# Kernel tuning notes

Hardware: AMD Instinct MI355X
Metric: run time of the kernel (lower is better)

Reference implementation:

```python
import jax, jax.numpy as jnp
import numpy as np

NUM_HEADS = 16
D_MODEL = 1024
HEAD_DIM = D_MODEL // NUM_HEADS
NEG_BIG = 1e10


def setup_inputs() -> dict:
    key = jax.random.key(0)
    k1, k2, k3 = jax.random.split(key, 3)
    B, T = 2, 2048
    from_tensor = jax.random.normal(k1, (B, T, D_MODEL), dtype=jnp.float32)
    init = 0.02
    Wqkv = jax.random.normal(k2, (D_MODEL, 3 * D_MODEL), dtype=jnp.float32) * init
    bqkv = jnp.zeros((3 * D_MODEL,), dtype=jnp.float32)
    Wproj = jax.random.normal(k3, (D_MODEL, D_MODEL), dtype=jnp.float32) * init
    bproj = jnp.zeros((D_MODEL,), dtype=jnp.float32)
    return {"from_tensor": from_tensor, "Wqkv": Wqkv, "bqkv": bqkv,
            "Wproj": Wproj, "bproj": bproj}


def reference(from_tensor, Wqkv, bqkv, Wproj, bproj):
    B, T, D = from_tensor.shape
    H, hd = NUM_HEADS, D // NUM_HEADS
    qkv = from_tensor @ Wqkv + bqkv                      # [B,T,3D]
    q, k, v = jnp.split(qkv, 3, axis=-1)
    def heads(x):  # [B,T,D] -> [B,H,T,hd]
        return x.reshape(B, T, H, hd).transpose(0, 2, 1, 3)
    q, k, v = heads(q), heads(k), heads(v)
    present = jnp.stack([k, v], axis=1)                  # [B,2,H,T,hd]
    scores = jnp.einsum('bhqd,bhkd->bhqk', q, k)         # [B,H,T,T]
    scores = scores * jax.lax.rsqrt(jnp.float32(hd))
    # faithful mask: m = i > j - ns + nd (strict; diagonal masked)
    nd = ns = T
    i = jnp.arange(nd)[:, None]
    j = jnp.arange(ns)
    m = (i > j - ns + nd).astype(scores.dtype)           # [T,T]
    scores = scores * m - NEG_BIG * (1.0 - m)
    probs = jax.nn.softmax(scores, axis=-1)
    ctx = jnp.einsum('bhqk,bhkd->bhqd', probs, v)        # [B,H,T,hd]
    ctx = ctx.transpose(0, 2, 1, 3).reshape(B, T, D)
    out = ctx @ Wproj + bproj                            # [B,T,D]
    return out, present
```

## Files before the change

### kernel.cpp

```cpp
#include <hip/hip_runtime.h>
#include <hip/hip_bf16.h>
#include <cstdint>

typedef __bf16 bf16_t;
typedef __bf16 bf16x4 __attribute__((ext_vector_type(4)));
typedef __bf16 bf16x8 __attribute__((ext_vector_type(8)));
typedef float  f32x4  __attribute__((ext_vector_type(4)));

#define MFMA16(a,b,c) __builtin_amdgcn_mfma_f32_16x16x32_bf16(a,b,c,0,0,0)

#if __has_builtin(__builtin_amdgcn_exp2f)
#define EXP2(x) __builtin_amdgcn_exp2f(x)
#else
#define EXP2(x) exp2f(x)
#endif

__device__ __forceinline__ void gl_lds16(const void* g, void* l){
    __builtin_amdgcn_global_load_lds(
        (const __attribute__((address_space(1))) void*)g,
        (__attribute__((address_space(3))) void*)l, 16, 0, 0);
}

__global__ void k_cvt(const float* __restrict__ src, bf16_t* __restrict__ dst, int n4){
    int stride = gridDim.x * blockDim.x;
    for (int i = blockIdx.x * blockDim.x + threadIdx.x; i < n4; i += stride){
        float4 v = ((const float4*)src)[i];
        bf16x4 o = { (bf16_t)v.x, (bf16_t)v.y, (bf16_t)v.z, (bf16_t)v.w };
        ((bf16x4*)dst)[i] = o;
    }
}

__global__ void k_transpose_cvt(const float* __restrict__ src, bf16_t* __restrict__ dst,
                                int R, int C){
    __shared__ bf16_t tile[32][33];
    int c0 = blockIdx.x * 32, r0 = blockIdx.y * 32;
    int tx = threadIdx.x & 31, g = threadIdx.x >> 5;
#pragma unroll
    for (int p = 0; p < 4; ++p){
        int r = g + p * 8;
        tile[r][tx] = (bf16_t)src[(size_t)(r0 + r) * C + c0 + tx];
    }
    __syncthreads();
#pragma unroll
    for (int p = 0; p < 4; ++p){
        int rr = g + p * 8;
        dst[(size_t)(c0 + rr) * R + r0 + tx] = tile[tx][rr];
    }
}

template<int MODE>
__global__ void k_gemm(const bf16_t* __restrict__ A, const bf16_t* __restrict__ Bt,
                       const float* __restrict__ bias,
                       float* __restrict__ Cout,
                       bf16_t* __restrict__ qws, bf16_t* __restrict__ kws,
                       bf16_t* __restrict__ vws,
                       int M, int N, int K){
    __shared__ bf16_t sA[128 * 64];
    __shared__ bf16_t sB[128 * 64];
    int m0 = blockIdx.x * 128, n0 = blockIdx.y * 128;
    int tid = threadIdx.x, lane = tid & 63, w = tid >> 6;
    int lr = lane & 15, lg = lane >> 4;
    int wm = (w >> 1) * 64, wn = (w & 1) * 64;
    f32x4 acc[4][4] = {};

    int srow = lane >> 3;
    int scol = ((lane & 7) ^ srow) * 8;

    for (int k0 = 0; k0 < K; k0 += 64){
#pragma unroll
        for (int p = 0; p < 4; ++p){
            int c = w + p * 4;
            gl_lds16(A  + (size_t)(m0 + c * 8 + srow) * K + k0 + scol, &sA[c * 512]);
            gl_lds16(Bt + (size_t)(n0 + c * 8 + srow) * K + k0 + scol, &sB[c * 512]);
        }
        __syncthreads();
#pragma unroll
        for (int ks = 0; ks < 2; ++ks){
            bf16x8 af[4], bfm[4];
            int ca = ((ks * 4 + lg) ^ (lr & 7)) * 8;
#pragma unroll
            for (int i = 0; i < 4; ++i){
                af[i]  = *(const bf16x8*)(sA + (wm + i * 16 + lr) * 64 + ca);
                bfm[i] = *(const bf16x8*)(sB + (wn + i * 16 + lr) * 64 + ca);
            }
            __builtin_amdgcn_s_setprio(1);
#pragma unroll
            for (int i = 0; i < 4; ++i)
#pragma unroll
                for (int j = 0; j < 4; ++j)
                    acc[i][j] = MFMA16(bfm[j], af[i], acc[i][j]);
            __builtin_amdgcn_s_setprio(0);
        }
        __syncthreads();
    }

#pragma unroll
    for (int j = 0; j < 4; ++j){
        int nb = n0 + wn + j * 16 + lg * 4;
        f32x4 bv = *(const f32x4*)(bias + nb);
#pragma unroll
        for (int i = 0; i < 4; ++i){
            int m = m0 + wm + i * 16 + lr;
            f32x4 cv = acc[i][j];
            cv[0] += bv[0]; cv[1] += bv[1]; cv[2] += bv[2]; cv[3] += bv[3];
            if (MODE == 1){
                *(f32x4*)(Cout + (size_t)m * N + nb) = cv;
            } else {
                int b = m >> 11, t = m & 2047;
                int sec = nb >> 10, rem = nb & 1023;
                int h = rem >> 6, d = rem & 63;
                size_t hbase = (((size_t)b * 16 + h) * 2048 + t) * 64;
                if (sec == 0){
                    bf16x4 qv = {(bf16_t)cv[0], (bf16_t)cv[1], (bf16_t)cv[2], (bf16_t)cv[3]};
                    *(bf16x4*)(qws + hbase + d) = qv;
                } else if (sec == 1){
                    bf16x4 kv = {(bf16_t)cv[0], (bf16_t)cv[1], (bf16_t)cv[2], (bf16_t)cv[3]};
                    *(bf16x4*)(kws + hbase + (d ^ ((t & 7) << 3))) = kv;
                    *(f32x4*)(Cout + ((((size_t)b * 2 + 0) * 16 + h) * 2048 + t) * 64 + d) = cv;
                } else {
                    *(f32x4*)(Cout + ((((size_t)b * 2 + 1) * 16 + h) * 2048 + t) * 64 + d) = cv;
                    int tl = t & 63;
                    int sp = (tl & 0x23) | ((tl & 0x0C) << 1) | ((tl & 0x10) >> 2);
#pragma unroll
                    for (int r = 0; r < 4; ++r){
                        int dd = d + r;
                        vws[(((size_t)b * 16 + h) * 64 + dd) * 2048 + (t & ~63)
                            + (sp ^ ((dd & 7) << 3))] = (bf16_t)cv[r];
                    }
                }
            }
        }
    }
}

__device__ __forceinline__ void stage_kv8(const bf16_t* khead, const bf16_t* vhead,
                                          bf16_t* sKb, bf16_t* sVb,
                                          int kv0, int w, int lane){
    gl_lds16(khead + (size_t)(kv0 + w * 8 + (lane >> 3)) * 64 + (lane & 7) * 8,
             sKb + w * 512);
    gl_lds16(vhead + (size_t)(w * 8 + (lane >> 3)) * 2048 + kv0 + (lane & 7) * 8,
             sVb + w * 512);
}

__global__ __launch_bounds__(512, 4) void k_flash(const bf16_t* __restrict__ qb,
                        const bf16_t* __restrict__ kb, const bf16_t* __restrict__ vt,
                        bf16_t* __restrict__ ctx){
    __shared__ bf16_t sK[3][4096];
    __shared__ bf16_t sV[3][4096];
    int bid = blockIdx.x;
    int x = bid & 7, p = bid >> 3;
    int c = p & 31, pass = p >> 5;
    int bh = x * 4 + pass * 2 + (c >> 4);
    int qt = pass ? 15 - (c & 15) : (c & 15);
    int b = bh >> 4, h = bh & 15;
    int tid = threadIdx.x, lane = tid & 63, w = tid >> 6;
    int lr = lane & 15, lg = lane >> 4;
    int q0 = qt * 128;
    int nkt = 2 * qt + 2;
    const bf16_t* qhead = qb + (size_t)bh * 131072;
    const bf16_t* khead = kb + (size_t)bh * 131072;
    const bf16_t* vhead = vt + (size_t)bh * 131072;
    const float SC = 0.18033688f;

    bf16x8 aq0, aq1;
    {
        const bf16_t* p2 = qhead + (size_t)(q0 + w * 16 + lr) * 64 + lg * 8;
        bf16x8 r0 = *(const bf16x8*)p2, r1 = *(const bf16x8*)(p2 + 32);
#pragma unroll
        for (int j = 0; j < 8; ++j){
            aq0[j] = (bf16_t)((float)r0[j] * SC);
            aq1[j] = (bf16_t)((float)r1[j] * SC);
        }
    }
    float lsum = 0.f;
    f32x4 oacc[4] = {};

    bf16_t *cK = sK[0], *cV = sV[0];
    bf16_t *nK = sK[1], *nV = sV[1];
    bf16_t *xK = sK[2], *xV = sV[2];
    stage_kv8(khead, vhead, cK, cV, 0, w, lane);
    stage_kv8(khead, vhead, nK, nV, 64, w, lane);

    for (int kt = 0; kt < nkt; ++kt){
        asm volatile("s_waitcnt vmcnt(2)" ::: "memory");
        __builtin_amdgcn_s_barrier();
        {
            int nt = kt + 2; if (nt > nkt - 1) nt = nkt - 1;
            stage_kv8(khead, vhead, xK, xV, nt * 64, w, lane);
        }

        bf16x8 kf[8], vf[8];
#pragma unroll
        for (int cf = 0; cf < 4; ++cf){
            kf[cf * 2]     = *(const bf16x8*)(&cK[(cf * 16 + lr) * 64 + ((lg * 8) ^ ((lr & 7) << 3))]);
            kf[cf * 2 + 1] = *(const bf16x8*)(&cK[(cf * 16 + lr) * 64 + ((32 + lg * 8) ^ ((lr & 7) << 3))]);
        }
#pragma unroll
        for (int ks = 0; ks < 2; ++ks)
#pragma unroll
            for (int df = 0; df < 4; ++df)
                vf[ks * 4 + df] = *(const bf16x8*)(&cV[(df * 16 + lr) * 64 + ((ks * 32 + lg * 8) ^ ((lr & 7) << 3))]);

        f32x4 s[4];
        __builtin_amdgcn_s_setprio(1);
#pragma unroll
        for (int cf = 0; cf < 4; ++cf){
            f32x4 a = {};
            a = MFMA16(kf[cf * 2],     aq0, a);
            a = MFMA16(kf[cf * 2 + 1], aq1, a);
            s[cf] = a;
        }
        __builtin_amdgcn_s_setprio(0);
        if (kt >= 2 * qt){
            int qi = q0 + w * 16 + lr;
            int kvg = kt * 64;
#pragma unroll
            for (int cf = 0; cf < 4; ++cf){
                int kvb = kvg + cf * 16 + lg * 4;
#pragma unroll
                for (int r = 0; r < 4; ++r)
                    if (qi <= kvb + r) s[cf][r] = -1e10f;
            }
        }
        __builtin_amdgcn_sched_barrier(0);
        float rsum = 0.f;
        bf16x8 ap0, ap1;
#pragma unroll
        for (int cf = 0; cf < 4; ++cf)
#pragma unroll
            for (int r = 0; r < 4; ++r){
                float pv = EXP2(s[cf][r]);
                rsum += pv;
                if (cf < 2) ap0[(cf & 1) * 4 + r] = (bf16_t)pv;
                else        ap1[(cf & 1) * 4 + r] = (bf16_t)pv;
            }
        lsum += rsum;
        __builtin_amdgcn_s_setprio(1);
#pragma unroll
        for (int ks = 0; ks < 2; ++ks){
            bf16x8 ap = ks ? ap1 : ap0;
#pragma unroll
            for (int df = 0; df < 4; ++df)
                oacc[df] = MFMA16(ap, vf[ks * 4 + df], oacc[df]);
        }
        __builtin_amdgcn_s_setprio(0);
        bf16_t* tK = cK; bf16_t* tV = cV;
        cK = nK; cV = nV; nK = xK; nV = xV; xK = tK; xV = tV;
    }
    asm volatile("s_waitcnt vmcnt(0)" ::: "memory");

    float lt = lsum;
    lt += __shfl_xor(lt, 16);
    lt += __shfl_xor(lt, 32);
    float ls0 = __shfl(lt, lg * 4 + 0);
    float ls1 = __shfl(lt, lg * 4 + 1);
    float ls2 = __shfl(lt, lg * 4 + 2);
    float ls3 = __shfl(lt, lg * 4 + 3);
#pragma unroll
    for (int df = 0; df < 4; ++df){
        int d = df * 16 + lr;
        int tb = q0 + w * 16 + lg * 4;
        size_t base = ((size_t)b * 2048 + tb) * 1024 + h * 64 + d;
        ctx[base]        = (bf16_t)(oacc[df][0] / ls0);
        ctx[base + 1024] = (bf16_t)(oacc[df][1] / ls1);
        ctx[base + 2048] = (bf16_t)(oacc[df][2] / ls2);
        ctx[base + 3072] = (bf16_t)(oacc[df][3] / ls3);
    }
}

__global__ void k_row0fix(const bf16_t* __restrict__ vt, bf16_t* __restrict__ ctx){
    int bh = blockIdx.y;
    int b = bh >> 4, h = bh & 15;
    int lane = threadIdx.x & 63, w = threadIdx.x >> 6;
    int d = blockIdx.x * 4 + w;
    const bf16_t* row = vt + ((size_t)bh * 64 + d) * 2048;
    float s = 0.f;
#pragma unroll
    for (int k = 0; k < 4; ++k){
        bf16x8 v = *(const bf16x8*)(row + (lane + k * 64) * 8);
#pragma unroll
        for (int j = 0; j < 8; ++j) s += (float)v[j];
    }
#pragma unroll
    for (int off = 1; off < 64; off <<= 1) s += __shfl_xor(s, off);
    if (lane == 0)
        ctx[(size_t)b * 2048 * 1024 + h * 64 + d] = (bf16_t)(s * (1.f / 2048.f));
}

extern "C" void kernel_launch(void* const* d_in, const int* in_sizes, int n_in,
                              void* d_out, int out_size, void* d_ws, size_t ws_size,
                              hipStream_t stream){
    const float* X     = (const float*)d_in[0];
    const float* Wqkv  = (const float*)d_in[1];
    const float* bqkv  = (const float*)d_in[2];
    const float* Wproj = (const float*)d_in[3];
    const float* bproj = (const float*)d_in[4];
    float* out = (float*)d_out;
    float* present = out + 4194304;

    char* ws = (char*)d_ws;
    bf16_t* Xb     = (bf16_t*)(ws);
    bf16_t* WqkvT  = (bf16_t*)(ws + 8388608);
    bf16_t* WprojT = (bf16_t*)(ws + 14680064);
    bf16_t* Qb     = (bf16_t*)(ws + 16777216);
    bf16_t* Kb     = (bf16_t*)(ws + 25165824);
    bf16_t* Vt     = (bf16_t*)(ws + 33554432);
    bf16_t* CTXb   = (bf16_t*)(ws + 41943040);

    k_cvt<<<2048, 256, 0, stream>>>(X, Xb, 4194304 / 4);
    k_transpose_cvt<<<dim3(3072 / 32, 1024 / 32), 256, 0, stream>>>(Wqkv, WqkvT, 1024, 3072);
    k_transpose_cvt<<<dim3(1024 / 32, 1024 / 32), 256, 0, stream>>>(Wproj, WprojT, 1024, 1024);
    k_gemm<0><<<dim3(32, 24), 256, 0, stream>>>(Xb, WqkvT, bqkv, present, Qb, Kb, Vt, 4096, 3072, 1024);
    k_flash<<<512, 512, 0, stream>>>(Qb, Kb, Vt, CTXb);
    k_row0fix<<<dim3(16, 32), 256, 0, stream>>>(Vt, CTXb);
    k_gemm<1><<<dim3(32, 8), 256, 0, stream>>>(CTXb, WprojT, bproj, out, nullptr, nullptr, nullptr, 4096, 1024, 1024);
}
```

Baseline: 99.74 us.

## Shrink flash tiles to 64 query rows with 4 waves and double-buffered KV

Each flash-attention block now handles 64 query rows with 4 waves (256 threads) instead of 128 rows with 8 waves, which doubles the grid to 1024 blocks. The block-to-(head, query-tile) mapping is changed to pair short and long causal tiles. The KV staging moves from a triple buffer with early prefetch to a double buffer refilled after a second barrier each iteration, and each wave now issues two loads per tile. The goals are finer load balance and lower LDS use per block, at the cost of an extra barrier per KV tile, less prefetch depth, and more total KV traffic because each K/V tile is reused by fewer query rows.

```diff
diff --git a/kernel.cpp b/kernel.cpp
--- a/kernel.cpp
+++ b/kernel.cpp
@@ -133,30 +133,34 @@
     }
 }
 
-__device__ __forceinline__ void stage_kv8(const bf16_t* khead, const bf16_t* vhead,
+__device__ __forceinline__ void stage_kv4(const bf16_t* khead, const bf16_t* vhead,
                                           bf16_t* sKb, bf16_t* sVb,
                                           int kv0, int w, int lane){
-    gl_lds16(khead + (size_t)(kv0 + w * 8 + (lane >> 3)) * 64 + (lane & 7) * 8,
-             sKb + w * 512);
-    gl_lds16(vhead + (size_t)(w * 8 + (lane >> 3)) * 2048 + kv0 + (lane & 7) * 8,
-             sVb + w * 512);
-}
-
-__global__ __launch_bounds__(512, 4) void k_flash(const bf16_t* __restrict__ qb,
+#pragma unroll
+    for (int p = 0; p < 2; ++p){
+        int c = w + p * 4;
+        gl_lds16(khead + (size_t)(kv0 + c * 8 + (lane >> 3)) * 64 + (lane & 7) * 8,
+                 sKb + c * 512);
+        gl_lds16(vhead + (size_t)(c * 8 + (lane >> 3)) * 2048 + kv0 + (lane & 7) * 8,
+                 sVb + c * 512);
+    }
+}
+
+__global__ __launch_bounds__(256, 4) void k_flash(const bf16_t* __restrict__ qb,
                         const bf16_t* __restrict__ kb, const bf16_t* __restrict__ vt,
                         bf16_t* __restrict__ ctx){
-    __shared__ bf16_t sK[3][4096];
-    __shared__ bf16_t sV[3][4096];
+    __shared__ bf16_t sK[2][4096];
+    __shared__ bf16_t sV[2][4096];
     int bid = blockIdx.x;
     int x = bid & 7, p = bid >> 3;
-    int c = p & 31, pass = p >> 5;
-    int bh = x * 4 + pass * 2 + (c >> 4);
-    int qt = pass ? 15 - (c & 15) : (c & 15);
+    int c = p & 31, layer = p >> 5;
+    int bh = x * 4 + layer;
+    int qt = (layer & 1) ? 31 - c : c;
     int b = bh >> 4, h = bh & 15;
     int tid = threadIdx.x, lane = tid & 63, w = tid >> 6;
     int lr = lane & 15, lg = lane >> 4;
-    int q0 = qt * 128;
-    int nkt = 2 * qt + 2;
+    int q0 = qt * 64;
+    int nkt = qt + 1;
     const bf16_t* qhead = qb + (size_t)bh * 131072;
     const bf16_t* khead = kb + (size_t)bh * 131072;
     const bf16_t* vhead = vt + (size_t)bh * 131072;
@@ -175,19 +179,14 @@
     float lsum = 0.f;
     f32x4 oacc[4] = {};
 
-    bf16_t *cK = sK[0], *cV = sV[0];
-    bf16_t *nK = sK[1], *nV = sV[1];
-    bf16_t *xK = sK[2], *xV = sV[2];
-    stage_kv8(khead, vhead, cK, cV, 0, w, lane);
-    stage_kv8(khead, vhead, nK, nV, 64, w, lane);
+    stage_kv4(khead, vhead, sK[0], sV[0], 0, w, lane);
+    stage_kv4(khead, vhead, sK[1], sV[1], (1 <= nkt - 1 ? 1 : 0) * 64, w, lane);
 
     for (int kt = 0; kt < nkt; ++kt){
-        asm volatile("s_waitcnt vmcnt(2)" ::: "memory");
+        asm volatile("s_waitcnt vmcnt(4)" ::: "memory");
         __builtin_amdgcn_s_barrier();
-        {
-            int nt = kt + 2; if (nt > nkt - 1) nt = nkt - 1;
-            stage_kv8(khead, vhead, xK, xV, nt * 64, w, lane);
-        }
+        const bf16_t* cK = sK[kt & 1];
+        const bf16_t* cV = sV[kt & 1];
 
         bf16x8 kf[8], vf[8];
 #pragma unroll
@@ -211,7 +210,7 @@
             s[cf] = a;
         }
         __builtin_amdgcn_s_setprio(0);
-        if (kt >= 2 * qt){
+        if (kt == nkt - 1){
             int qi = q0 + w * 16 + lr;
             int kvg = kt * 64;
 #pragma unroll
@@ -244,8 +243,11 @@
                 oacc[df] = MFMA16(ap, vf[ks * 4 + df], oacc[df]);
         }
         __builtin_amdgcn_s_setprio(0);
-        bf16_t* tK = cK; bf16_t* tV = cV;
-        cK = nK; cV = nV; nK = xK; nV = xV; xK = tK; xV = tV;
+        __builtin_amdgcn_s_barrier();
+        {
+            int nt = kt + 2; if (nt > nkt - 1) nt = nkt - 1;
+            stage_kv4(khead, vhead, sK[kt & 1], sV[kt & 1], nt * 64, w, lane);
+        }
     }
     asm volatile("s_waitcnt vmcnt(0)" ::: "memory");
 
@@ -311,7 +313,7 @@
     k_transpose_cvt<<<dim3(3072 / 32, 1024 / 32), 256, 0, stream>>>(Wqkv, WqkvT, 1024, 3072);
     k_transpose_cvt<<<dim3(1024 / 32, 1024 / 32), 256, 0, stream>>>(Wproj, WprojT, 1024, 1024);
     k_gemm<0><<<dim3(32, 24), 256, 0, stream>>>(Xb, WqkvT, bqkv, present, Qb, Kb, Vt, 4096, 3072, 1024);
-    k_flash<<<512, 512, 0, stream>>>(Qb, Kb, Vt, CTXb);
+    k_flash<<<1024, 256, 0, stream>>>(Qb, Kb, Vt, CTXb);
     k_row0fix<<<dim3(16, 32), 256, 0, stream>>>(Vt, CTXb);
     k_gemm<1><<<dim3(32, 8), 256, 0, stream>>>(CTXb, WprojT, bproj, out, nullptr, nullptr, nullptr, 4096, 1024, 1024);
 }
```

New measurement: 106.9 us. 1.07x slower.
